# Kernel optimization log

Hardware: AMD Instinct MI355X
Metric: run time of the kernel (lower is better)

Reference implementation:

```python
import jax, jax.numpy as jnp
import numpy as np

B, S, D, P, NQ = 8, 2048, 1024, 256, 8192


def setup_inputs() -> dict:
    key = jax.random.key(0)
    ks = jax.random.split(key, 8)
    return {
        "flag": 0,
        "encoded_input": jax.random.normal(ks[0], (B, S, D), dtype=jnp.float32),
        "start_ids_1": jax.random.randint(ks[1], (NQ,), 0, S, dtype=jnp.int32),
        "end_ids_1": jax.random.randint(ks[2], (NQ,), 0, S, dtype=jnp.int32),
        "query_batch_idx": jax.random.randint(ks[3], (NQ,), 0, B, dtype=jnp.int32),
        "start_ids_2": jax.random.randint(ks[4], (NQ,), 0, S, dtype=jnp.int32),
        "end_ids_2": jax.random.randint(ks[5], (NQ,), 0, S, dtype=jnp.int32),
        "W": jax.random.normal(ks[6], (D, P), dtype=jnp.float32) * 0.02,
        "b": jnp.zeros((P,), dtype=jnp.float32),
    }


def _gather_spans(h, qb, s, e):
    # span_repr[b, i, j] = concat(h[b, i], h[b, j]) for j >= i, else 0.
    # Direct gather instead of building the O(seq^2) table.
    rep = jnp.concatenate([h[qb, s], h[qb, e]], axis=-1)  # [NQ, 2*P]
    valid = (e >= s).astype(rep.dtype)[:, None]
    return rep * valid


def reference(flag, encoded_input, start_ids_1, end_ids_1, query_batch_idx,
              start_ids_2, end_ids_2, W, b):
    h = encoded_input @ W + b  # [B, S, P] (use_proj=True)
    res1 = _gather_spans(h, query_batch_idx, start_ids_1, end_ids_1)
    res2 = _gather_spans(h, query_batch_idx, start_ids_2, end_ids_2)
    return (res1, res2)
```

## Files before the change

kernel.cpp:

```cpp
#include <hip/hip_runtime.h>
#include <hip/hip_bf16.h>
#include <stdint.h>

#define S_LEN 2048
#define D_DIM 1024
#define P_DIM 256
#define NQ_   8192
#define M_TOT 16384

#define BM 64
#define BN 256
#define BK 64
#define CAP 32
#define HS  260

typedef __attribute__((ext_vector_type(4))) float  f32x4;
typedef __attribute__((ext_vector_type(8))) __bf16 bf16x8;

__device__ __forceinline__ void async16(const void* g, void* l) {
    __builtin_amdgcn_global_load_lds(
        (const __attribute__((address_space(1))) uint32_t*)g,
        (__attribute__((address_space(3))) uint32_t*)l, 16, 0, 0);
}

__global__ __launch_bounds__(1024) void wt_kernel(const float* __restrict__ W,
                                                  __bf16* __restrict__ WT,
                                                  int* __restrict__ cnt) {
    __shared__ __bf16 tile[32][33];
    const int k0 = blockIdx.x * 32;
    const int n0 = blockIdx.y * 32;
    const int tx = threadIdx.x, ty = threadIdx.y;
    const int g = (blockIdx.y * gridDim.x + blockIdx.x) * 1024 + ty * 32 + tx;
    if (g < M_TOT) cnt[g] = 0;
    tile[ty][tx] = (__bf16)W[(k0 + ty) * P_DIM + (n0 + tx)];
    __syncthreads();
    WT[(n0 + ty) * D_DIM + (k0 + tx)] = tile[tx][ty];
}

__global__ __launch_bounds__(256) void index_zero(const int* __restrict__ s1,
                                                  const int* __restrict__ e1,
                                                  const int* __restrict__ s2,
                                                  const int* __restrict__ e2,
                                                  const int* __restrict__ qb,
                                                  int* __restrict__ cnt,
                                                  int* __restrict__ bucket,
                                                  float* __restrict__ out) {
    const int q    = blockIdx.x * 256 + threadIdx.x;
    const int lane = threadIdx.x & 63;
    const int bqw  = blockIdx.x * 256 + (threadIdx.x & ~63);
    const int b    = qb[q];
    const float4 z = make_float4(0.f, 0.f, 0.f, 0.f);
    #pragma unroll
    for (int set = 0; set < 2; ++set) {
        const int s = set ? s2[q] : s1[q];
        const int e = set ? e2[q] : e1[q];
        if (e >= s) {
            int r = b * S_LEN + s;
            int k = atomicAdd(&cnt[r], 1); if (k < CAP) bucket[r * CAP + k] = (q << 2) | (set << 1);
            r = b * S_LEN + e;
            k = atomicAdd(&cnt[r], 1);     if (k < CAP) bucket[r * CAP + k] = (q << 2) | (set << 1) | 1;
        }
        unsigned long long mask = __ballot(e < s);
        while (mask) {
            const int j = __ffsll(mask) - 1;
            mask &= mask - 1;
            const int qz = bqw + j;
            float4* dst = (float4*)(out + (size_t)set * (NQ_ * 512) + (size_t)qz * 512);
            dst[lane]      = z;
            dst[lane + 64] = z;
        }
    }
}

__global__ __launch_bounds__(256, 1) void gemm_kernel(const float*  __restrict__ A,
                                                      const __bf16* __restrict__ WT,
                                                      const float*  __restrict__ bias,
                                                      const int*    __restrict__ cnt,
                                                      const int*    __restrict__ bucket,
                                                      float*        __restrict__ out) {
    __shared__ __align__(16) char smem[2 * BM * BK * 2 + 3 * BN * BK * 2];
    __shared__ int s_cnt[64];
    __shared__ int s_off[65];
    __shared__ int elist[64 * CAP];

    const int tid = threadIdx.x;
    const int w   = tid >> 6;
    const int l   = tid & 63;
    const int lm  = l & 15;
    const int q   = l >> 4;

    const int m0 = blockIdx.x * BM;

    auto bufA = [&](int buf) -> __bf16* { return (__bf16*)smem + buf * (BM * BK); };
    auto bufB = [&](int buf) -> __bf16* { return (__bf16*)(smem + 2 * BM * BK * 2) + buf * (BN * BK); };

    const int brow_l = l >> 3;
    const int bc     = (l & 7) ^ (brow_l & 7);

    auto stageB = [&](int buf, int k0) {
        __bf16* B = bufB(buf);
        #pragma unroll
        for (int j = 0; j < 8; ++j) {
            const int r   = w * 8 + j;
            const int row = r * 8 + brow_l;
            const __bf16* g = WT + (size_t)row * D_DIM + k0 + bc * 8;
            async16(g, B + r * 512);
        }
    };

    const int arow = tid >> 2;
    const int ac   = tid & 3;
    const float* agp = A + (size_t)(m0 + arow) * D_DIM + ac * 16;
    const int p0 = ((2 * ac)     ^ (arow & 7)) * 8;
    const int p1 = ((2 * ac + 1) ^ (arow & 7)) * 8;

    float4 fa[4];
    auto loadA = [&](int k0) {
        #pragma unroll
        for (int i = 0; i < 4; ++i) fa[i] = *(const float4*)(agp + k0 + 4 * i);
    };
    auto writeA = [&](int buf) {
        bf16x8 v0, v1;
        v0[0] = (__bf16)fa[0].x; v0[1] = (__bf16)fa[0].y; v0[2] = (__bf16)fa[0].z; v0[3] = (__bf16)fa[0].w;
        v0[4] = (__bf16)fa[1].x; v0[5] = (__bf16)fa[1].y; v0[6] = (__bf16)fa[1].z; v0[7] = (__bf16)fa[1].w;
        v1[0] = (__bf16)fa[2].x; v1[1] = (__bf16)fa[2].y; v1[2] = (__bf16)fa[2].z; v1[3] = (__bf16)fa[2].w;
        v1[4] = (__bf16)fa[3].x; v1[5] = (__bf16)fa[3].y; v1[6] = (__bf16)fa[3].z; v1[7] = (__bf16)fa[3].w;
        __bf16* Ab = bufA(buf) + arow * BK;
        *(bf16x8*)(Ab + p0) = v0;
        *(bf16x8*)(Ab + p1) = v1;
    };

    f32x4 acc[4][4] = {};

    auto compute = [&](int bufa, int bufb) {
        const __bf16* Ab = bufA(bufa);
        const __bf16* Bb = bufB(bufb);
        #pragma unroll
        for (int kh = 0; kh < 2; ++kh) {
            const int pos = ((kh * 4 + q) ^ (lm & 7)) * 8;
            bf16x8 af[4], bfr[4];
            #pragma unroll
            for (int mi = 0; mi < 4; ++mi)
                af[mi] = *(const bf16x8*)(Ab + (mi * 16 + lm) * BK + pos);
            #pragma unroll
            for (int ni = 0; ni < 4; ++ni)
                bfr[ni] = *(const bf16x8*)(Bb + (w * 64 + ni * 16 + lm) * BK + pos);
            #pragma unroll
            for (int mi = 0; mi < 4; ++mi)
                #pragma unroll
                for (int ni = 0; ni < 4; ++ni)
                    acc[mi][ni] = __builtin_amdgcn_mfma_f32_16x16x32_bf16(
                        af[mi], bfr[ni], acc[mi][ni], 0, 0, 0);
        }
    };

    loadA(0);
    stageB(0, 0);
    stageB(1, BK);
    writeA(0);
    loadA(BK);
    asm volatile("s_waitcnt lgkmcnt(0)");
    __builtin_amdgcn_sched_barrier(0);

    #pragma unroll 1
    for (int i = 0; i < 16; ++i) {
        __builtin_amdgcn_sched_barrier(0);
        if (i == 0)       asm volatile("s_waitcnt vmcnt(12)");
        else if (i == 15) asm volatile("s_waitcnt vmcnt(0)");
        else              asm volatile("s_waitcnt vmcnt(16)");
        __builtin_amdgcn_s_barrier();
        __builtin_amdgcn_sched_barrier(0);
        if (i <= 13) stageB((i + 2) % 3, (i + 2) * BK);
        __builtin_amdgcn_sched_barrier(0);
        compute(i & 1, i % 3);
        __builtin_amdgcn_sched_barrier(0);
        if (i <= 14) writeA((i + 1) & 1);
        if (i <= 13) loadA((i + 2) * BK);
        asm volatile("s_waitcnt lgkmcnt(0)");
        __builtin_amdgcn_sched_barrier(0);
    }

    __syncthreads();
    float* hs = (float*)smem;

    if (tid < 64) { int c = cnt[m0 + tid]; s_cnt[tid] = c < CAP ? c : CAP; }

    #pragma unroll
    for (int ni = 0; ni < 4; ++ni) {
        const int col = w * 64 + ni * 16 + lm;
        const float bv = bias[col];
        #pragma unroll
        for (int mi = 0; mi < 4; ++mi) {
            const int rbase = mi * 16 + q * 4;
            #pragma unroll
            for (int r = 0; r < 4; ++r)
                hs[(rbase + r) * HS + col] = acc[mi][ni][r] + bv;
        }
    }
    __syncthreads();
    if (tid == 0) {
        int a = 0;
        #pragma unroll 1
        for (int i = 0; i < 64; ++i) { s_off[i] = a; a += s_cnt[i]; }
        s_off[64] = a;
    }
    __syncthreads();
    if (tid < 64) {
        const int o = s_off[tid], c = s_cnt[tid];
        const int* bk = bucket + (size_t)(m0 + tid) * CAP;
        for (int k = 0; k < c; ++k)
            elist[o + k] = (tid << 15) | (bk[k] & 0x7fff);
    }
    __syncthreads();

    const int E   = s_off[64];
    const int grp = tid >> 6;
    const int gl  = tid & 63;
    #pragma unroll 1
    for (int j = grp; j < E; j += 4) {
        const int ent  = elist[j];
        const int rl   = ent >> 15;
        const int code = ent & 0x7fff;
        const int qq   = code >> 2;
        const int st   = (code >> 1) & 1;
        const int hf   = code & 1;
        const float4 v = *(const float4*)&hs[rl * HS + gl * 4];
        *(float4*)(out + (size_t)st * (NQ_ * 512) + (size_t)qq * 512 + hf * 256 + gl * 4) = v;
    }
}

extern "C" void kernel_launch(void* const* d_in, const int* in_sizes, int n_in,
                              void* d_out, int out_size, void* d_ws, size_t ws_size,
                              hipStream_t stream) {
    const float* A    = (const float*)d_in[1];
    const int*   s1   = (const int*)  d_in[2];
    const int*   e1   = (const int*)  d_in[3];
    const int*   qb   = (const int*)  d_in[4];
    const int*   s2   = (const int*)  d_in[5];
    const int*   e2   = (const int*)  d_in[6];
    const float* W    = (const float*)d_in[7];
    const float* bias = (const float*)d_in[8];
    float*       out  = (float*)d_out;

    __bf16* WT     = (__bf16*)d_ws;
    int*    cnt    = (int*)((char*)d_ws + (1 << 20));
    int*    bucket = (int*)((char*)d_ws + (1 << 20) + (1 << 16));

    wt_kernel  <<<dim3(32, 8), dim3(32, 32), 0, stream>>>(W, WT, cnt);
    index_zero <<<dim3(NQ_ / 256), dim3(256), 0, stream>>>(s1, e1, s2, e2, qb, cnt, bucket, out);
    gemm_kernel<<<dim3(M_TOT / BM), dim3(256), 0, stream>>>(A, WT, bias, cnt, bucket, out);
}
```

Before: 148.9 us.

## Pre-pack A and W into MFMA fragment layout and load GEMM operands directly to registers

Adds a separate conversion kernel that casts the fp32 activations to bf16 in a fragment-major layout, and changes the weight transpose to emit the same fragment layout. The GEMM then skips LDS staging and barriers, loading operand fragments straight from global memory into registers with a two-stage register double buffer. The M tile shrinks from 64 to 32 rows to allow two blocks per CU. The cost is an extra bf16 round trip of the full activation matrix through HBM, plus more redundant global reads of W because there is no LDS sharing across waves.

```diff
diff --git a/kernel.cpp b/kernel.cpp
--- a/kernel.cpp
+++ b/kernel.cpp
@@ -7,34 +7,56 @@
 #define P_DIM 256
 #define NQ_   8192
 #define M_TOT 16384
-
-#define BM 64
-#define BN 256
-#define BK 64
 #define CAP 32
 #define HS  260
 
 typedef __attribute__((ext_vector_type(4))) float  f32x4;
 typedef __attribute__((ext_vector_type(8))) __bf16 bf16x8;
 
-__device__ __forceinline__ void async16(const void* g, void* l) {
-    __builtin_amdgcn_global_load_lds(
-        (const __attribute__((address_space(1))) uint32_t*)g,
-        (__attribute__((address_space(3))) uint32_t*)l, 16, 0, 0);
-}
-
-__global__ __launch_bounds__(1024) void wt_kernel(const float* __restrict__ W,
-                                                  __bf16* __restrict__ WT,
-                                                  int* __restrict__ cnt) {
-    __shared__ __bf16 tile[32][33];
-    const int k0 = blockIdx.x * 32;
-    const int n0 = blockIdx.y * 32;
+
+__global__ __launch_bounds__(1024) void wtf_kernel(const float* __restrict__ W,
+                                                   __bf16* __restrict__ WTf,
+                                                   int* __restrict__ cnt) {
+    __shared__ float tile[32][33];
+    const int bx = blockIdx.x;
+    const int by = blockIdx.y;
+    const int k0 = bx * 32, n0 = by * 32;
     const int tx = threadIdx.x, ty = threadIdx.y;
-    const int g = (blockIdx.y * gridDim.x + blockIdx.x) * 1024 + ty * 32 + tx;
+    const int g = (by * 32 + bx) * 1024 + ty * 32 + tx;
     if (g < M_TOT) cnt[g] = 0;
-    tile[ty][tx] = (__bf16)W[(k0 + ty) * P_DIM + (n0 + tx)];
-    __syncthreads();
-    WT[(n0 + ty) * D_DIM + (k0 + tx)] = tile[tx][ty];
+    tile[ty][tx] = W[(k0 + ty) * P_DIM + (n0 + tx)];
+    __syncthreads();
+    const int t = ty * 32 + tx;
+    if (t < 128) {
+        const int c16r = t >> 6, q = (t >> 4) & 3, lm = t & 15;
+        bf16x8 v;
+        #pragma unroll
+        for (int e = 0; e < 8; ++e) v[e] = (__bf16)tile[q * 8 + e][c16r * 16 + lm];
+        const int c16 = by * 2 + c16r;
+        const int ts  = bx >> 1, kh = bx & 1;
+        *(bf16x8*)(WTf + (size_t)((c16 * 32 + ts * 2 + kh) * 512 + (q * 16 + lm) * 8)) = v;
+    }
+}
+
+__global__ __launch_bounds__(256) void a_cvt(const float* __restrict__ A,
+                                             __bf16* __restrict__ Af) {
+    const int b  = blockIdx.x;
+    const int t  = threadIdx.x;
+    const int rr = t >> 4;
+    const int cq = t & 15;
+    const float* src = A  + (size_t)(b * 16 + rr) * D_DIM;
+    __bf16*      dst = Af + (size_t)b * 16384;
+    #pragma unroll
+    for (int it = 0; it < 8; ++it) {
+        const int c = it * 16 + cq;
+        const float4 x0 = *(const float4*)(src + c * 8);
+        const float4 x1 = *(const float4*)(src + c * 8 + 4);
+        bf16x8 v;
+        v[0] = (__bf16)x0.x; v[1] = (__bf16)x0.y; v[2] = (__bf16)x0.z; v[3] = (__bf16)x0.w;
+        v[4] = (__bf16)x1.x; v[5] = (__bf16)x1.y; v[6] = (__bf16)x1.z; v[7] = (__bf16)x1.w;
+        const int ts = c >> 3, kh = (c >> 2) & 1, qp = c & 3;
+        *(bf16x8*)(dst + (ts * 2 + kh) * 512 + (qp * 16 + rr) * 8) = v;
+    }
 }
 
 __global__ __launch_bounds__(256) void index_zero(const int* __restrict__ s1,
@@ -72,16 +94,16 @@
     }
 }
 
-__global__ __launch_bounds__(256, 1) void gemm_kernel(const float*  __restrict__ A,
-                                                      const __bf16* __restrict__ WT,
+__global__ __launch_bounds__(256, 2) void gemm_kernel(const __bf16* __restrict__ Af,
+                                                      const __bf16* __restrict__ WTf,
                                                       const float*  __restrict__ bias,
                                                       const int*    __restrict__ cnt,
                                                       const int*    __restrict__ bucket,
                                                       float*        __restrict__ out) {
-    __shared__ __align__(16) char smem[2 * BM * BK * 2 + 3 * BN * BK * 2];
-    __shared__ int s_cnt[64];
-    __shared__ int s_off[65];
-    __shared__ int elist[64 * CAP];
+    __shared__ float hs[32 * HS];
+    __shared__ int s_cnt[32];
+    __shared__ int s_off[33];
+    __shared__ int elist[32 * CAP];
 
     const int tid = threadIdx.x;
     const int w   = tid >> 6;
@@ -89,108 +111,63 @@
     const int lm  = l & 15;
     const int q   = l >> 4;
 
-    const int m0 = blockIdx.x * BM;
-
-    auto bufA = [&](int buf) -> __bf16* { return (__bf16*)smem + buf * (BM * BK); };
-    auto bufB = [&](int buf) -> __bf16* { return (__bf16*)(smem + 2 * BM * BK * 2) + buf * (BN * BK); };
-
-    const int brow_l = l >> 3;
-    const int bc     = (l & 7) ^ (brow_l & 7);
-
-    auto stageB = [&](int buf, int k0) {
-        __bf16* B = bufB(buf);
-        #pragma unroll
-        for (int j = 0; j < 8; ++j) {
-            const int r   = w * 8 + j;
-            const int row = r * 8 + brow_l;
-            const __bf16* g = WT + (size_t)row * D_DIM + k0 + bc * 8;
-            async16(g, B + r * 512);
-        }
-    };
-
-    const int arow = tid >> 2;
-    const int ac   = tid & 3;
-    const float* agp = A + (size_t)(m0 + arow) * D_DIM + ac * 16;
-    const int p0 = ((2 * ac)     ^ (arow & 7)) * 8;
-    const int p1 = ((2 * ac + 1) ^ (arow & 7)) * 8;
-
-    float4 fa[4];
-    auto loadA = [&](int k0) {
-        #pragma unroll
-        for (int i = 0; i < 4; ++i) fa[i] = *(const float4*)(agp + k0 + 4 * i);
-    };
-    auto writeA = [&](int buf) {
-        bf16x8 v0, v1;
-        v0[0] = (__bf16)fa[0].x; v0[1] = (__bf16)fa[0].y; v0[2] = (__bf16)fa[0].z; v0[3] = (__bf16)fa[0].w;
-        v0[4] = (__bf16)fa[1].x; v0[5] = (__bf16)fa[1].y; v0[6] = (__bf16)fa[1].z; v0[7] = (__bf16)fa[1].w;
-        v1[0] = (__bf16)fa[2].x; v1[1] = (__bf16)fa[2].y; v1[2] = (__bf16)fa[2].z; v1[3] = (__bf16)fa[2].w;
-        v1[4] = (__bf16)fa[3].x; v1[5] = (__bf16)fa[3].y; v1[6] = (__bf16)fa[3].z; v1[7] = (__bf16)fa[3].w;
-        __bf16* Ab = bufA(buf) + arow * BK;
-        *(bf16x8*)(Ab + p0) = v0;
-        *(bf16x8*)(Ab + p1) = v1;
-    };
-
-    f32x4 acc[4][4] = {};
-
-    auto compute = [&](int bufa, int bufb) {
-        const __bf16* Ab = bufA(bufa);
-        const __bf16* Bb = bufB(bufb);
-        #pragma unroll
-        for (int kh = 0; kh < 2; ++kh) {
-            const int pos = ((kh * 4 + q) ^ (lm & 7)) * 8;
-            bf16x8 af[4], bfr[4];
-            #pragma unroll
-            for (int mi = 0; mi < 4; ++mi)
-                af[mi] = *(const bf16x8*)(Ab + (mi * 16 + lm) * BK + pos);
-            #pragma unroll
-            for (int ni = 0; ni < 4; ++ni)
-                bfr[ni] = *(const bf16x8*)(Bb + (w * 64 + ni * 16 + lm) * BK + pos);
-            #pragma unroll
-            for (int mi = 0; mi < 4; ++mi)
-                #pragma unroll
-                for (int ni = 0; ni < 4; ++ni)
-                    acc[mi][ni] = __builtin_amdgcn_mfma_f32_16x16x32_bf16(
-                        af[mi], bfr[ni], acc[mi][ni], 0, 0, 0);
-        }
-    };
-
-    loadA(0);
-    stageB(0, 0);
-    stageB(1, BK);
-    writeA(0);
-    loadA(BK);
-    asm volatile("s_waitcnt lgkmcnt(0)");
-    __builtin_amdgcn_sched_barrier(0);
-
+    const int m0  = blockIdx.x * 32;
+    const int r16 = blockIdx.x * 2;
+
+    const __bf16* apb[2][2];
+    const __bf16* bpb[4][2];
+    #pragma unroll
+    for (int mi = 0; mi < 2; ++mi)
+        #pragma unroll
+        for (int kh = 0; kh < 2; ++kh)
+            apb[mi][kh] = Af + (size_t)(((r16 + mi) * 32 + kh) * 512 + l * 8);
+    #pragma unroll
+    for (int ni = 0; ni < 4; ++ni)
+        #pragma unroll
+        for (int kh = 0; kh < 2; ++kh)
+            bpb[ni][kh] = WTf + (size_t)(((w * 4 + ni) * 32 + kh) * 512 + l * 8);
+
+    bf16x8 a_[2][2][2];
+    bf16x8 b_[2][4][2];
+    f32x4  acc[2][4] = {};
+
+#define LOADSTEP(B, T)                                                        \
+    _Pragma("unroll") for (int mi = 0; mi < 2; ++mi)                          \
+        _Pragma("unroll") for (int kh = 0; kh < 2; ++kh)                      \
+            a_[B][mi][kh] = *(const bf16x8*)(apb[mi][kh] + (T) * 1024);       \
+    _Pragma("unroll") for (int ni = 0; ni < 4; ++ni)                          \
+        _Pragma("unroll") for (int kh = 0; kh < 2; ++kh)                      \
+            b_[B][ni][kh] = *(const bf16x8*)(bpb[ni][kh] + (T) * 1024);
+
+#define MMASTEP(B)                                                            \
+    _Pragma("unroll") for (int kh = 0; kh < 2; ++kh)                          \
+        _Pragma("unroll") for (int mi = 0; mi < 2; ++mi)                      \
+            _Pragma("unroll") for (int ni = 0; ni < 4; ++ni)                  \
+                acc[mi][ni] = __builtin_amdgcn_mfma_f32_16x16x32_bf16(        \
+                    a_[B][mi][kh], b_[B][ni][kh], acc[mi][ni], 0, 0, 0);
+
+    LOADSTEP(0, 0)
     #pragma unroll 1
-    for (int i = 0; i < 16; ++i) {
-        __builtin_amdgcn_sched_barrier(0);
-        if (i == 0)       asm volatile("s_waitcnt vmcnt(12)");
-        else if (i == 15) asm volatile("s_waitcnt vmcnt(0)");
-        else              asm volatile("s_waitcnt vmcnt(16)");
-        __builtin_amdgcn_s_barrier();
-        __builtin_amdgcn_sched_barrier(0);
-        if (i <= 13) stageB((i + 2) % 3, (i + 2) * BK);
-        __builtin_amdgcn_sched_barrier(0);
-        compute(i & 1, i % 3);
-        __builtin_amdgcn_sched_barrier(0);
-        if (i <= 14) writeA((i + 1) & 1);
-        if (i <= 13) loadA((i + 2) * BK);
-        asm volatile("s_waitcnt lgkmcnt(0)");
-        __builtin_amdgcn_sched_barrier(0);
-    }
-
-    __syncthreads();
-    float* hs = (float*)smem;
-
-    if (tid < 64) { int c = cnt[m0 + tid]; s_cnt[tid] = c < CAP ? c : CAP; }
+    for (int t = 0; t < 14; t += 2) {
+        LOADSTEP(1, t + 1)
+        MMASTEP(0)
+        LOADSTEP(0, t + 2)
+        MMASTEP(1)
+    }
+    LOADSTEP(1, 15)
+    MMASTEP(0)
+    MMASTEP(1)
+#undef LOADSTEP
+#undef MMASTEP
+
+    if (tid < 32) { int c = cnt[m0 + tid]; s_cnt[tid] = c < CAP ? c : CAP; }
 
     #pragma unroll
     for (int ni = 0; ni < 4; ++ni) {
         const int col = w * 64 + ni * 16 + lm;
         const float bv = bias[col];
         #pragma unroll
-        for (int mi = 0; mi < 4; ++mi) {
+        for (int mi = 0; mi < 2; ++mi) {
             const int rbase = mi * 16 + q * 4;
             #pragma unroll
             for (int r = 0; r < 4; ++r)
@@ -201,11 +178,11 @@
     if (tid == 0) {
         int a = 0;
         #pragma unroll 1
-        for (int i = 0; i < 64; ++i) { s_off[i] = a; a += s_cnt[i]; }
-        s_off[64] = a;
-    }
-    __syncthreads();
-    if (tid < 64) {
+        for (int i = 0; i < 32; ++i) { s_off[i] = a; a += s_cnt[i]; }
+        s_off[32] = a;
+    }
+    __syncthreads();
+    if (tid < 32) {
         const int o = s_off[tid], c = s_cnt[tid];
         const int* bk = bucket + (size_t)(m0 + tid) * CAP;
         for (int k = 0; k < c; ++k)
@@ -213,7 +190,7 @@
     }
     __syncthreads();
 
-    const int E   = s_off[64];
+    const int E   = s_off[32];
     const int grp = tid >> 6;
     const int gl  = tid & 63;
     #pragma unroll 1
@@ -242,11 +219,13 @@
     const float* bias = (const float*)d_in[8];
     float*       out  = (float*)d_out;
 
-    __bf16* WT     = (__bf16*)d_ws;
+    __bf16* WTf    = (__bf16*)d_ws;
     int*    cnt    = (int*)((char*)d_ws + (1 << 20));
     int*    bucket = (int*)((char*)d_ws + (1 << 20) + (1 << 16));
-
-    wt_kernel  <<<dim3(32, 8), dim3(32, 32), 0, stream>>>(W, WT, cnt);
+    __bf16* Af     = (__bf16*)((char*)d_ws + (16 << 20));
+
+    a_cvt      <<<dim3(1024), dim3(256), 0, stream>>>(A, Af);
+    wtf_kernel <<<dim3(32, 8), dim3(32, 32), 0, stream>>>(W, WTf, cnt);
     index_zero <<<dim3(NQ_ / 256), dim3(256), 0, stream>>>(s1, e1, s2, e2, qb, cnt, bucket, out);
-    gemm_kernel<<<dim3(M_TOT / BM), dim3(256), 0, stream>>>(A, WT, bias, cnt, bucket, out);
-}
+    gemm_kernel<<<dim3(M_TOT / 32), dim3(256), 0, stream>>>(Af, WTf, bias, cnt, bucket, out);
+}
```

Result: slower. 154.1 us (+3.5%).
